# Kernel optimization log

Measured on AMD Instinct MI355X. Metric: run time of the kernel, lower is better.

## Reference

```python
import jax, jax.numpy as jnp
import numpy as np

S = 2048        # sequence length
D_MODEL = 1024  # model dim
H = 16          # mqa_n_queries
D = 64          # mqa_query_dim
WIN = 128       # mqa_window


def setup_inputs() -> dict:
    key = jax.random.key(0)
    ks = jax.random.split(key, 5)
    scale_in = 1.0 / np.sqrt(D_MODEL)
    return {
        "x": jax.random.normal(ks[0], (S, D_MODEL), dtype=jnp.float32),
        "Wqkv": jax.random.normal(ks[1], (D * (H + 2), D_MODEL), dtype=jnp.float32) * scale_in,
        "bqkv": jax.random.normal(ks[2], (D * (H + 2),), dtype=jnp.float32) * 0.01,
        "Wout": jax.random.normal(ks[3], (D_MODEL, D_MODEL), dtype=jnp.float32) * scale_in,
        "bout": jax.random.normal(ks[4], (D_MODEL,), dtype=jnp.float32) * 0.01,
    }


def reference(x, Wqkv, bqkv, Wout, bout):
    seq = x.shape[0]
    # fused QKV projection: 1 shared K, 1 shared V, H query heads (MQA)
    qkv = x @ Wqkv.T + bqkv                        # (S, D*(H+2))
    k = qkv[:, :D]                                 # (S, D) shared key
    v = qkv[:, D:2 * D]                            # (S, D) shared value
    q = qkv[:, 2 * D:].reshape(seq, H, D)          # (S, H, D)

    i = jnp.arange(seq)[:, None]
    j = jnp.arange(seq)[None, :]
    mask = (j <= i) & (j > i - WIN)                # (S, S)

    # NOTE: original multiplies by sqrt(D) (not 1/sqrt(D)); kept faithful.
    scores = jnp.sqrt(jnp.float32(D)) * jnp.einsum('ihd,jd->hij', q, k)  # (H, S, S)
    scores = jnp.where(mask, scores, -jnp.inf)
    attn = jax.nn.softmax(scores, axis=-1)         # every row has >=1 valid entry

    o = jnp.einsum('hij,jd->ihd', attn, v).reshape(seq, H * D)  # (S, d_model)
    return o @ Wout.T + bout
```

## Files before the change

kernel.cpp:

```cpp
#include <hip/hip_runtime.h>
#include <math.h>

#define S_LEN 2048
#define DMODEL 1024
#define NHEAD 16
#define DHEAD 64
#define WIN 128
#define NQKV 1152

typedef _Float16 f16x8 __attribute__((ext_vector_type(8)));
typedef float f32x4 __attribute__((ext_vector_type(4)));

__device__ __forceinline__ ushort f2h(float f) {
  union { _Float16 h; ushort u; } v; v.h = (_Float16)f; return v.u;
}

typedef __attribute__((address_space(1))) const unsigned GU;
typedef __attribute__((address_space(3))) unsigned LU;
__device__ __forceinline__ void async16(const ushort* g, ushort* l) {
  __builtin_amdgcn_global_load_lds((GU*)g, (LU*)l, 16, 0, 0);
}

__global__ __launch_bounds__(256)
void convert_kernel(const float4* __restrict__ x, const float4* __restrict__ wq,
                    ushort4* __restrict__ x16, ushort4* __restrict__ w16) {
  const int NX4 = (S_LEN * DMODEL) / 4;
  const int i = blockIdx.x * 256 + threadIdx.x;
  if (i < NX4) {
    const float4 v = x[i];
    ushort4 h; h.x = f2h(v.x); h.y = f2h(v.y); h.z = f2h(v.z); h.w = f2h(v.w);
    x16[i] = h;
  } else {
    const int j = i - NX4;
    const float s = ((j >> 8) >= 2 * DHEAD) ? 8.0f : 1.0f;
    const float4 v = wq[j];
    ushort4 h; h.x = f2h(v.x * s); h.y = f2h(v.y * s); h.z = f2h(v.z * s); h.w = f2h(v.w * s);
    w16[j] = h;
  }
}

template<int MODE>
__global__ __launch_bounds__(256)
void gemm32(const ushort* __restrict__ A, const ushort* __restrict__ B,
            const float* __restrict__ bias, float* __restrict__ Cout,
            ushort* __restrict__ k16, ushort* __restrict__ vT, ushort* __restrict__ q16,
            int M, int N, int K) {
  __shared__ __align__(16) ushort sA[2][32 * 64];
  __shared__ __align__(16) ushort sB[2][64 * 64];
  const int t = threadIdx.x;
  const int w = t >> 6, lane = t & 63;
  const int quad = lane >> 4, l16 = lane & 15;
  const int wn = w * 16;

  const int bid = blockIdx.x;
  const int half = (N >> 6) >> 1;
  const int xcd = bid & 7, l = bid >> 3;
  const int mg = xcd >> 1, ng = xcd & 1;
  const int m0 = (mg * 16 + (l & 15)) * 32;
  const int n0 = (ng * half + (l >> 4)) * 64;

  const int lr = lane >> 3;
  const int lc = (lane & 7) ^ lr;
  const size_t aBase = (size_t)(m0 + 8 * w + lr) * K + lc * 8;
  const size_t bBase = (size_t)(n0 + 16 * w + lr) * K + lc * 8;

  f32x4 acc[2] = {};

  auto STAGE = [&](int ktile, int b) {
    const size_t koff = (size_t)ktile << 6;
    async16(A + aBase + koff, &sA[b][(8 * w) * 64]);
#pragma unroll
    for (int i = 0; i < 2; ++i)
      async16(B + bBase + (size_t)(8 * i) * K + koff, &sB[b][(16 * w + 8 * i) * 64]);
  };

  STAGE(0, 0);
  __syncthreads();

  const int NT = K >> 6;
  for (int kt = 0; kt < NT; ++kt) {
    const int cur = kt & 1;
    if (kt + 1 < NT) STAGE(kt + 1, cur ^ 1);

    f16x8 af[2][2], bf[2];
#pragma unroll
    for (int kst = 0; kst < 2; ++kst) {
      const int cp = ((kst << 2) | quad) ^ (l16 & 7);
#pragma unroll
      for (int i = 0; i < 2; ++i)
        af[kst][i] = *(const f16x8*)(&sA[cur][(16 * i + l16) * 64 + cp * 8]);
      bf[kst] = *(const f16x8*)(&sB[cur][(wn + l16) * 64 + cp * 8]);
    }
#pragma unroll
    for (int kst = 0; kst < 2; ++kst)
#pragma unroll
      for (int i = 0; i < 2; ++i)
        acc[i] = __builtin_amdgcn_mfma_f32_16x16x32_f16(af[kst][i], bf[kst], acc[i], 0, 0, 0);
    __syncthreads();
  }

  const int cb = n0 + wn;
  const int col = cb + l16;
#pragma unroll
  for (int i = 0; i < 2; ++i) {
    if (MODE == 0) {
      const float b = bias[col];
#pragma unroll
      for (int r = 0; r < 4; ++r) {
        const int row = m0 + 16 * i + quad * 4 + r;
        Cout[(size_t)row * N + col] = acc[i][r] + b;
      }
    } else {
      const float bscale = (cb >= 2 * DHEAD) ? 8.0f : 1.0f;
      const float b = bias[col] * bscale;
#pragma unroll
      for (int r = 0; r < 4; ++r) {
        const int row = m0 + 16 * i + quad * 4 + r;
        const ushort h = f2h(acc[i][r] + b);
        if (cb >= 2 * DHEAD) {
          q16[(size_t)row * DMODEL + (col - 2 * DHEAD)] = h;
        } else if (cb < DHEAD) {
          k16[(size_t)row * DHEAD + col] = h;
        } else {
          vT[(size_t)(col - DHEAD) * S_LEN + row] = h;
        }
      }
    }
  }
}

#define QT 4
#define NTK 10
#define KST 5
#define PSTR 176

__global__ __launch_bounds__(256)
void attn_kernel(const ushort* __restrict__ k16, const ushort* __restrict__ vT,
                 const ushort* __restrict__ q16, ushort* __restrict__ obuf,
                 const float4* __restrict__ wo, ushort4* __restrict__ wo16) {
  __shared__ __align__(16) ushort lds[64 * PSTR + 64 * PSTR];
  ushort* Ksw = lds;
  ushort* P   = lds;
  ushort* Vt  = lds + 64 * PSTR;

  const int t = threadIdx.x;
  const int i0 = blockIdx.x * QT;
  const int jbase = (i0 >= WIN - 1) ? ((i0 - (WIN - 1)) & ~7) : 0;
  const int w = t >> 6, lane = t & 63;
  const int quad = lane >> 4, l16 = lane & 15;
  const int qg = i0 + w;

#pragma unroll
  for (int i = 0; i < 5; ++i) {
    const int n = 5 * w + i;
    const int r = 8 * n + (lane >> 3);
    const int cs = (lane & 7) ^ (r & 7);
    async16(k16 + (size_t)(jbase + r) * DHEAD + cs * 8, &Ksw[n * 512]);
  }
  {
    const int base = blockIdx.x * 512 + t;
#pragma unroll
    for (int u = 0; u < 2; ++u) {
      const int idx = base + u * 256;
      const float4 v = wo[idx];
      ushort4 h; h.x = f2h(v.x); h.y = f2h(v.y); h.z = f2h(v.z); h.w = f2h(v.w);
      wo16[idx] = h;
    }
  }
  {
    const int d = t >> 2, p = t & 3;
#pragma unroll
    for (int it = 0; it < 5; ++it) {
      const int c = p + 4 * it;
      const uint4 raw = *(const uint4*)(vT + (size_t)d * S_LEN + jbase + c * 8);
      *(uint4*)(&Vt[d * PSTR + c * 8]) = raw;
    }
  }
  f16x8 qf[2];
  {
    const size_t qbase = (size_t)qg * DMODEL + l16 * DHEAD;
#pragma unroll
    for (int kst = 0; kst < 2; ++kst)
      qf[kst] = *(const f16x8*)(q16 + qbase + kst * 32 + quad * 8);
  }
  __syncthreads();

  f32x4 acc[NTK] = {};
#pragma unroll
  for (int nt = 0; nt < NTK; ++nt) {
#pragma unroll
    for (int kst = 0; kst < 2; ++kst) {
      const int cp = ((kst << 2) | quad) ^ (l16 & 7);
      const f16x8 bf = *(const f16x8*)(&Ksw[(nt * 16 + l16) * 64 + cp * 8]);
      acc[nt] = __builtin_amdgcn_mfma_f32_16x16x32_f16(qf[kst], bf, acc[nt], 0, 0, 0);
    }
  }
  __syncthreads();

  float inv_l[4];
#pragma unroll
  for (int nt = 0; nt < NTK; ++nt) {
    const int jg = jbase + nt * 16 + l16;
    const bool valid = (jg <= qg) && (jg > qg - WIN);
#pragma unroll
    for (int r = 0; r < 4; ++r)
      if (!valid) acc[nt][r] = -1e30f;
  }
#pragma unroll
  for (int r = 0; r < 4; ++r) {
    float m = acc[0][r];
#pragma unroll
    for (int nt = 1; nt < NTK; ++nt) m = fmaxf(m, acc[nt][r]);
#pragma unroll
    for (int off = 1; off < 16; off <<= 1) m = fmaxf(m, __shfl_xor(m, off));
    float s = 0.f;
#pragma unroll
    for (int nt = 0; nt < NTK; ++nt) {
      const float e = __expf(acc[nt][r] - m);
      acc[nt][r] = e;
      s += e;
    }
#pragma unroll
    for (int off = 1; off < 16; off <<= 1) s += __shfl_xor(s, off);
    inv_l[r] = 1.0f / s;
  }
  {
    const int mrow0 = w * 16 + quad * 4;
#pragma unroll
    for (int r = 0; r < 4; ++r)
#pragma unroll
      for (int nt = 0; nt < NTK; ++nt)
        P[(mrow0 + r) * PSTR + nt * 16 + l16] = f2h(acc[nt][r]);
  }
  __syncthreads();

  f32x4 o[4] = {};
#pragma unroll
  for (int kst = 0; kst < KST; ++kst) {
    const f16x8 a = *(const f16x8*)(&P[(w * 16 + l16) * PSTR + kst * 32 + quad * 8]);
#pragma unroll
    for (int nd = 0; nd < 4; ++nd) {
      const f16x8 b = *(const f16x8*)(&Vt[(nd * 16 + l16) * PSTR + kst * 32 + quad * 8]);
      o[nd] = __builtin_amdgcn_mfma_f32_16x16x32_f16(a, b, o[nd], 0, 0, 0);
    }
  }

  {
    const size_t obase = (size_t)qg * DMODEL;
#pragma unroll
    for (int nd = 0; nd < 4; ++nd)
#pragma unroll
      for (int r = 0; r < 4; ++r) {
        const int col = (quad * 4 + r) * DHEAD + nd * 16 + l16;
        obuf[obase + col] = f2h(o[nd][r] * inv_l[r]);
      }
  }
}

extern "C" void kernel_launch(void* const* d_in, const int* in_sizes, int n_in,
                              void* d_out, int out_size, void* d_ws, size_t ws_size,
                              hipStream_t stream) {
  const float* x    = (const float*)d_in[0];
  const float* Wqkv = (const float*)d_in[1];
  const float* bqkv = (const float*)d_in[2];
  const float* Wout = (const float*)d_in[3];
  const float* bout = (const float*)d_in[4];
  float* out = (float*)d_out;

  char* w = (char*)d_ws;
  ushort* x16  = (ushort*)(w + 0);
  ushort* w16  = (ushort*)(w + 4194304);
  ushort* wo16 = (ushort*)(w + 6553600);
  ushort* k16  = (ushort*)(w + 8650752);
  ushort* vT   = (ushort*)(w + 8921088);
  ushort* q16  = (ushort*)(w + 9191424);
  ushort* obuf = (ushort*)(w + 13385728);

  convert_kernel<<<3200, 256, 0, stream>>>(
      (const float4*)x, (const float4*)Wqkv, (ushort4*)x16, (ushort4*)w16);

  gemm32<1><<<1152, 256, 0, stream>>>(x16, w16, bqkv, nullptr, k16, vT, q16,
                                      S_LEN, NQKV, DMODEL);

  attn_kernel<<<S_LEN / QT, 256, 0, stream>>>(k16, vT, q16, obuf,
                                              (const float4*)Wout, (ushort4*)wo16);

  gemm32<0><<<1024, 256, 0, stream>>>(obuf, wo16, bout, out, nullptr, nullptr, nullptr,
                                      S_LEN, DMODEL, DMODEL);
}
```

Before: 105.4 us.

## Fuse fp32-to-fp16 conversion of x and Wqkv into the QKV GEMM

Drops the separate conversion kernel. The QKV GEMM now loads fp32 x and Wqkv straight into registers, converts them to fp16 (applying the x8 query-weight scale per row), and stores them into the swizzled LDS tiles. The write for the next tile happens after the current MFMAs, replacing the async global-to-LDS copies. This removes a kernel launch and the fp16 intermediate write and re-read. In exchange, each GEMM tile reads twice as many bytes, with synchronous register staging instead of async LDS loads, and the conversion is redone for every reuse of an A or B tile.

Result: slower. 110.5 us (+4.8%).

```diff
diff --git a/kernel.cpp b/kernel.cpp
--- a/kernel.cpp
+++ b/kernel.cpp
@@ -21,27 +21,10 @@
   __builtin_amdgcn_global_load_lds((GU*)g, (LU*)l, 16, 0, 0);
 }
 
-__global__ __launch_bounds__(256)
-void convert_kernel(const float4* __restrict__ x, const float4* __restrict__ wq,
-                    ushort4* __restrict__ x16, ushort4* __restrict__ w16) {
-  const int NX4 = (S_LEN * DMODEL) / 4;
-  const int i = blockIdx.x * 256 + threadIdx.x;
-  if (i < NX4) {
-    const float4 v = x[i];
-    ushort4 h; h.x = f2h(v.x); h.y = f2h(v.y); h.z = f2h(v.z); h.w = f2h(v.w);
-    x16[i] = h;
-  } else {
-    const int j = i - NX4;
-    const float s = ((j >> 8) >= 2 * DHEAD) ? 8.0f : 1.0f;
-    const float4 v = wq[j];
-    ushort4 h; h.x = f2h(v.x * s); h.y = f2h(v.y * s); h.z = f2h(v.z * s); h.w = f2h(v.w * s);
-    w16[j] = h;
-  }
-}
-
 template<int MODE>
 __global__ __launch_bounds__(256)
-void gemm32(const ushort* __restrict__ A, const ushort* __restrict__ B,
+void gemm32(const ushort* __restrict__ A16, const ushort* __restrict__ B16,
+            const float* __restrict__ A32, const float* __restrict__ B32,
             const float* __restrict__ bias, float* __restrict__ Cout,
             ushort* __restrict__ k16, ushort* __restrict__ vT, ushort* __restrict__ q16,
             int M, int N, int K) {
@@ -65,38 +48,86 @@
   const size_t bBase = (size_t)(n0 + 16 * w + lr) * K + lc * 8;
 
   f32x4 acc[2] = {};
-
-  auto STAGE = [&](int ktile, int b) {
-    const size_t koff = (size_t)ktile << 6;
-    async16(A + aBase + koff, &sA[b][(8 * w) * 64]);
-#pragma unroll
-    for (int i = 0; i < 2; ++i)
-      async16(B + bBase + (size_t)(8 * i) * K + koff, &sB[b][(16 * w + 8 * i) * 64]);
-  };
-
-  STAGE(0, 0);
-  __syncthreads();
-
   const int NT = K >> 6;
-  for (int kt = 0; kt < NT; ++kt) {
-    const int cur = kt & 1;
-    if (kt + 1 < NT) STAGE(kt + 1, cur ^ 1);
-
-    f16x8 af[2][2], bf[2];
-#pragma unroll
-    for (int kst = 0; kst < 2; ++kst) {
-      const int cp = ((kst << 2) | quad) ^ (l16 & 7);
+
+  if (MODE == 0) {
+    auto STAGE = [&](int ktile, int b) {
+      const size_t koff = (size_t)ktile << 6;
+      async16(A16 + aBase + koff, &sA[b][(8 * w) * 64]);
 #pragma unroll
       for (int i = 0; i < 2; ++i)
-        af[kst][i] = *(const f16x8*)(&sA[cur][(16 * i + l16) * 64 + cp * 8]);
-      bf[kst] = *(const f16x8*)(&sB[cur][(wn + l16) * 64 + cp * 8]);
-    }
-#pragma unroll
-    for (int kst = 0; kst < 2; ++kst)
-#pragma unroll
-      for (int i = 0; i < 2; ++i)
-        acc[i] = __builtin_amdgcn_mfma_f32_16x16x32_f16(af[kst][i], bf[kst], acc[i], 0, 0, 0);
+        async16(B16 + bBase + (size_t)(8 * i) * K + koff, &sB[b][(16 * w + 8 * i) * 64]);
+    };
+    STAGE(0, 0);
     __syncthreads();
+    for (int kt = 0; kt < NT; ++kt) {
+      const int cur = kt & 1;
+      if (kt + 1 < NT) STAGE(kt + 1, cur ^ 1);
+      f16x8 af[2][2], bf[2];
+#pragma unroll
+      for (int kst = 0; kst < 2; ++kst) {
+        const int cp = ((kst << 2) | quad) ^ (l16 & 7);
+#pragma unroll
+        for (int i = 0; i < 2; ++i)
+          af[kst][i] = *(const f16x8*)(&sA[cur][(16 * i + l16) * 64 + cp * 8]);
+        bf[kst] = *(const f16x8*)(&sB[cur][(wn + l16) * 64 + cp * 8]);
+      }
+#pragma unroll
+      for (int kst = 0; kst < 2; ++kst)
+#pragma unroll
+        for (int i = 0; i < 2; ++i)
+          acc[i] = __builtin_amdgcn_mfma_f32_16x16x32_f16(af[kst][i], bf[kst], acc[i], 0, 0, 0);
+      __syncthreads();
+    }
+  } else {
+    const float bsc0 = (n0 + 16 * w + lr >= 2 * DHEAD) ? 8.0f : 1.0f;
+    const float bsc1 = (n0 + 16 * w + 8 + lr >= 2 * DHEAD) ? 8.0f : 1.0f;
+    float4 ra[2], rb0[2], rb1[2];
+    auto LOAD = [&](int ktile) {
+      const size_t koff = (size_t)ktile << 6;
+      ra[0]  = *(const float4*)(A32 + aBase + koff);
+      ra[1]  = *(const float4*)(A32 + aBase + koff + 4);
+      rb0[0] = *(const float4*)(B32 + bBase + koff);
+      rb0[1] = *(const float4*)(B32 + bBase + koff + 4);
+      rb1[0] = *(const float4*)(B32 + bBase + (size_t)8 * K + koff);
+      rb1[1] = *(const float4*)(B32 + bBase + (size_t)8 * K + koff + 4);
+    };
+    auto CVT = [&](const float4* r, float s) -> f16x8 {
+      f16x8 h;
+      h[0] = (_Float16)(r[0].x * s); h[1] = (_Float16)(r[0].y * s);
+      h[2] = (_Float16)(r[0].z * s); h[3] = (_Float16)(r[0].w * s);
+      h[4] = (_Float16)(r[1].x * s); h[5] = (_Float16)(r[1].y * s);
+      h[6] = (_Float16)(r[1].z * s); h[7] = (_Float16)(r[1].w * s);
+      return h;
+    };
+    auto WRITE = [&](int b) {
+      *(f16x8*)(&sA[b][(8 * w + lr) * 64 + (lane & 7) * 8])        = CVT(ra, 1.0f);
+      *(f16x8*)(&sB[b][(16 * w + lr) * 64 + (lane & 7) * 8])       = CVT(rb0, bsc0);
+      *(f16x8*)(&sB[b][(16 * w + 8 + lr) * 64 + (lane & 7) * 8])   = CVT(rb1, bsc1);
+    };
+    LOAD(0);
+    WRITE(0);
+    __syncthreads();
+    for (int kt = 0; kt < NT; ++kt) {
+      const int cur = kt & 1;
+      if (kt + 1 < NT) LOAD(kt + 1);
+      f16x8 af[2][2], bf[2];
+#pragma unroll
+      for (int kst = 0; kst < 2; ++kst) {
+        const int cp = ((kst << 2) | quad) ^ (l16 & 7);
+#pragma unroll
+        for (int i = 0; i < 2; ++i)
+          af[kst][i] = *(const f16x8*)(&sA[cur][(16 * i + l16) * 64 + cp * 8]);
+        bf[kst] = *(const f16x8*)(&sB[cur][(wn + l16) * 64 + cp * 8]);
+      }
+#pragma unroll
+      for (int kst = 0; kst < 2; ++kst)
+#pragma unroll
+        for (int i = 0; i < 2; ++i)
+          acc[i] = __builtin_amdgcn_mfma_f32_16x16x32_f16(af[kst][i], bf[kst], acc[i], 0, 0, 0);
+      if (kt + 1 < NT) WRITE(cur ^ 1);
+      __syncthreads();
+    }
   }
 
   const int cb = n0 + wn;
@@ -268,23 +299,18 @@
   float* out = (float*)d_out;
 
   char* w = (char*)d_ws;
-  ushort* x16  = (ushort*)(w + 0);
-  ushort* w16  = (ushort*)(w + 4194304);
   ushort* wo16 = (ushort*)(w + 6553600);
   ushort* k16  = (ushort*)(w + 8650752);
   ushort* vT   = (ushort*)(w + 8921088);
   ushort* q16  = (ushort*)(w + 9191424);
   ushort* obuf = (ushort*)(w + 13385728);
 
-  convert_kernel<<<3200, 256, 0, stream>>>(
-      (const float4*)x, (const float4*)Wqkv, (ushort4*)x16, (ushort4*)w16);
-
-  gemm32<1><<<1152, 256, 0, stream>>>(x16, w16, bqkv, nullptr, k16, vT, q16,
-                                      S_LEN, NQKV, DMODEL);
+  gemm32<1><<<1152, 256, 0, stream>>>(nullptr, nullptr, x, Wqkv, bqkv, nullptr,
+                                      k16, vT, q16, S_LEN, NQKV, DMODEL);
 
   attn_kernel<<<S_LEN / QT, 256, 0, stream>>>(k16, vT, q16, obuf,
                                               (const float4*)Wout, (ushort4*)wo16);
 
-  gemm32<0><<<1024, 256, 0, stream>>>(obuf, wo16, bout, out, nullptr, nullptr, nullptr,
-                                      S_LEN, DMODEL, DMODEL);
-}
+  gemm32<0><<<1024, 256, 0, stream>>>(obuf, wo16, nullptr, nullptr, bout, out,
+                                      nullptr, nullptr, nullptr, S_LEN, DMODEL, DMODEL);
+}
```
